# Kernel tuning notes

Hardware: AMD Instinct MI355X
Metric: run time of the kernel (lower is better)

Reference implementation:

```python
import jax, jax.numpy as jnp
import numpy as np

N = 50000          # nodes
E = 800000         # edges (no self loops; self loops added in reference)
D = 128            # in_channels == out_channels (required by index_add into x)
HEADS = 1
NEG_SLOPE = 0.2
NUM_LABELS = 7


def setup_inputs() -> dict:
    key = jax.random.key(0)
    k0, k1, k2, k3, k4, k5 = jax.random.split(key, 6)
    x = jax.random.normal(k0, (N, D), dtype=jnp.float32)
    # edges guaranteed self-loop-free (remove_self_loops is then a no-op)
    src = jax.random.randint(k1, (E,), 0, N, dtype=jnp.int32)
    off = jax.random.randint(k2, (E,), 1, N, dtype=jnp.int32)
    dst = (src + off) % N
    edge_index = jnp.stack([src, dst])  # [2, E]
    node_label = jax.random.randint(k3, (N,), 0, 8, dtype=jnp.int32)  # 0 = inactive, 1..7 active
    glorot = float(np.sqrt(6.0 / (D + D)))
    weight_id = jax.random.uniform(k4, (NUM_LABELS, D, D), jnp.float32, -glorot, glorot)
    ga = float(np.sqrt(6.0 / (HEADS * 2 * D + 1)))
    att = jax.random.uniform(k5, (1, HEADS, 2 * D), jnp.float32, -ga, ga)
    return {"x": x, "edge_index": edge_index, "node_label": node_label,
            "weight_id": weight_id, "att": att}


def reference(x, edge_index, node_label, weight_id, att):
    n, d = x.shape
    # --- per-label identity transform: ox = x + W_{label-1} x for labels 1..7 ---
    y = jnp.einsum('nd,kdo->nko', x, weight_id)           # [N, 7, D]
    valid = (node_label >= 1) & (node_label <= NUM_LABELS)
    idx = jnp.clip(node_label - 1, 0, NUM_LABELS - 1)
    delta = jnp.take_along_axis(y, idx[:, None, None], axis=1)[:, 0]  # [N, D]
    ox = x + jnp.where(valid[:, None], delta, jnp.zeros_like(delta))
    # --- add self loops (input has none) ---
    loops = jnp.arange(n, dtype=edge_index.dtype)
    src = jnp.concatenate([edge_index[0], loops])
    dst = jnp.concatenate([edge_index[1], loops])
    # --- GAT message: gather, attention score, edge softmax over dst ---
    x_j = ox[src].reshape(-1, HEADS, d)                   # [Et, 1, D]
    x_i = ox[dst].reshape(-1, HEADS, d)
    alpha = (x_i * att[:, :, :d]).sum(-1) + (x_j * att[:, :, d:]).sum(-1)  # [Et, 1]
    alpha = jax.nn.leaky_relu(alpha, NEG_SLOPE)
    amax = jax.ops.segment_max(alpha, dst, num_segments=n)  # every node has a self loop
    alpha = jnp.exp(alpha - amax[dst])
    denom = jax.ops.segment_sum(alpha, dst, num_segments=n)
    alpha = alpha / (denom[dst] + 1e-16)
    # dropout p=0 (eval) -> no-op
    msg = (x_j * alpha[:, :, None]).reshape(-1, HEADS * d)  # concat=True, heads=1
    out = jax.ops.segment_sum(msg, dst, num_segments=n)     # [N, D]; bias=False
    return out
```

## Files before the change

### kernel.cpp

```cpp
#include <hip/hip_runtime.h>
#include <math.h>

#define N_NODES 50000
#define N_EDGES 800000
#define DIM 128
#define DEG_CAP 48
#define BINS ((N_NODES + 255) / 256)
#define BIN_CAP 8192
#define EA_CHUNK 3125
#define BA_BLOCKS ((N_EDGES + EA_CHUNK - 1) / EA_CHUNK)
#define EA_UNR 13

#define LB_BLOCKS ((N_NODES + 255) / 256)
#define WT_BLOCKS ((7 * DIM * DIM + 255) / 256)
#define K1_GRID (BA_BLOCKS + LB_BLOCKS + WT_BLOCKS)

#define TR_TILES 3133
#define K2_GRID (BINS + TR_TILES)

#define XS_STRIDE 132

typedef __attribute__((ext_vector_type(8))) short short8;
typedef __attribute__((ext_vector_type(4))) float floatx4;

__device__ __forceinline__ unsigned short f2bf(float f) {
    unsigned int u = __float_as_uint(f);
    unsigned int r = (u + 0x7fff + ((u >> 16) & 1)) >> 16;
    return (unsigned short)r;
}
__device__ __forceinline__ float bf2f_lo(unsigned int v) { return __uint_as_float(v << 16); }
__device__ __forceinline__ float bf2f_hi(unsigned int v) { return __uint_as_float(v & 0xffff0000u); }

__global__ __launch_bounds__(256) void build_kernel(
        const int* __restrict__ src, const int* __restrict__ dst,
        const int* __restrict__ label, const float* __restrict__ W,
        unsigned short* __restrict__ Wt,
        int* __restrict__ bin_cur, unsigned int* __restrict__ binned,
        int* __restrict__ lab_cnt, int* __restrict__ node_list) {
    int t = threadIdx.x;
    int blk = blockIdx.x;

    if (blk < BA_BLOCKS) {
        __shared__ int hist[BINS], base_s[BINS], rank[BINS];
        for (int i = t; i < BINS; i += 256) { hist[i] = 0; rank[i] = 0; }
        __syncthreads();
        int e0 = blk * EA_CHUNK;
        int e1 = e0 + EA_CHUNK; if (e1 > N_EDGES) e1 = N_EDGES;
        int dl[EA_UNR];
        #pragma unroll
        for (int k = 0; k < EA_UNR; k++) {
            int e = e0 + t + k * 256;
            dl[k] = (e < e1) ? dst[e] : -1;
        }
        #pragma unroll
        for (int k = 0; k < EA_UNR; k++)
            if (dl[k] >= 0) atomicAdd(&hist[dl[k] >> 8], 1);
        __syncthreads();
        for (int i = t; i < BINS; i += 256)
            base_s[i] = (hist[i] > 0) ? atomicAdd(&bin_cur[i], hist[i]) : 0;
        __syncthreads();
        int sl[EA_UNR];
        #pragma unroll
        for (int k = 0; k < EA_UNR; k++) {
            int e = e0 + t + k * 256;
            sl[k] = (e < e1) ? src[e] : 0;
        }
        #pragma unroll
        for (int k = 0; k < EA_UNR; k++) {
            if (dl[k] >= 0) {
                int d = dl[k];
                int b = d >> 8;
                int r = atomicAdd(&rank[b], 1);
                int slot = base_s[b] + r;
                if (slot < BIN_CAP)
                    binned[(size_t)b * BIN_CAP + slot] = (unsigned int)(sl[k] | ((d & 255) << 16));
            }
        }
    } else if (blk < BA_BLOCKS + LB_BLOCKS) {
        __shared__ int lcnt[8], lbase[8], lrank[8];
        int i = (blk - BA_BLOCKS) * 256 + t;
        if (t < 8) { lcnt[t] = 0; lrank[t] = 0; }
        __syncthreads();
        int b = -1;
        if (i < N_NODES) {
            int lab = label[i];
            b = (lab >= 1 && lab <= 7) ? (lab - 1) : 7;
            atomicAdd(&lcnt[b], 1);
        }
        __syncthreads();
        if (t < 8) lbase[t] = (lcnt[t] > 0) ? atomicAdd(&lab_cnt[t], lcnt[t]) : 0;
        __syncthreads();
        if (i < N_NODES) {
            int r = atomicAdd(&lrank[b], 1);
            node_list[(size_t)b * N_NODES + lbase[b] + r] = i;
        }
    } else {
        int j = (blk - BA_BLOCKS - LB_BLOCKS) * 256 + t;
        if (j < 7 * DIM * DIM) {
            int b = j >> 14;
            int d = (j >> 7) & 127;
            int c = j & 127;
            Wt[((size_t)b * DIM + c) * DIM + d] = f2bf(W[j]);
        }
    }
}

__global__ __launch_bounds__(256) void phase2_kernel(
        const float* __restrict__ x, const float* __restrict__ att,
        const int* __restrict__ lab_cnt, const int* __restrict__ node_list,
        const unsigned short* __restrict__ Wt,
        const int* __restrict__ bin_cur, const unsigned int* __restrict__ binned,
        unsigned short* __restrict__ oxh, float* __restrict__ ai, float* __restrict__ aj,
        int* __restrict__ cnt, unsigned short* __restrict__ bucket) {
    __shared__ __align__(16) char smem[25600];
    int t = threadIdx.x;
    int blk = blockIdx.x;

    if (blk < BINS) {
        unsigned short (*rows)[DEG_CAP] = (unsigned short (*)[DEG_CAP])smem;
        int* lcnt = (int*)(smem + 24576);
        int b = blk;
        int m = bin_cur[b]; if (m > BIN_CAP) m = BIN_CAP;
        const unsigned int* bp = binned + (size_t)b * BIN_CAP;

        lcnt[t] = 0;
        __syncthreads();
        for (int i0 = 0; i0 < m; i0 += 1024) {
            unsigned int v[4];
            #pragma unroll
            for (int u = 0; u < 4; u++) {
                int i = i0 + u * 256 + t;
                v[u] = (i < m) ? bp[i] : 0u;
            }
            #pragma unroll
            for (int u = 0; u < 4; u++) {
                int i = i0 + u * 256 + t;
                if (i < m) {
                    int ln = (v[u] >> 16) & 255;
                    int p = atomicAdd(&lcnt[ln], 1);
                    if (p < DEG_CAP) rows[ln][p] = (unsigned short)(v[u] & 0xFFFF);
                }
            }
        }
        __syncthreads();
        int n = b * 256 + t;
        if (n < N_NODES) {
            int deg = lcnt[t];
            if (deg > DEG_CAP) deg = DEG_CAP;
            cnt[n] = deg;
        }
        uint4* gdst = (uint4*)(bucket + (size_t)b * 256 * DEG_CAP);
        const uint4* lsrc = (const uint4*)rows;
        #pragma unroll
        for (int k = 0; k < (256 * DEG_CAP * 2 / 16) / 256; k++)
            gdst[t + k * 256] = lsrc[t + k * 256];
    } else {
        int tile = blk - BINS;
        int b = 0, base = 0, tcnt = 0;
        for (; b < 8; b++) {
            int c = lab_cnt[b];
            int nt = (c + 15) >> 4;
            if (tile < nt) { base = b * N_NODES + tile * 16; tcnt = c - tile * 16; break; }
            tile -= nt;
        }
        if (b == 8) return;
        if (tcnt > 16) tcnt = 16;

        float* xs  = (float*)smem;
        float* red = (float*)(smem + 16 * XS_STRIDE * 4);

        {
            const float4* x4 = (const float4*)x;
            int j = t;
            #pragma unroll
            for (int k = 0; k < 2; k++, j += 256) {
                int row = j >> 5;
                int c4  = j & 31;
                int node = node_list[base + ((row < tcnt) ? row : 0)];
                float4 v = x4[(size_t)node * 32 + c4];
                *(float4*)(xs + row * XS_STRIDE + c4 * 4) = v;
            }
        }
        __syncthreads();

        int wv = t >> 6;
        int lane = t & 63;
        int m = lane & 15;
        int quad = lane >> 4;

        floatx4 acc[2];
        acc[0] = (floatx4){0.f, 0.f, 0.f, 0.f};
        acc[1] = (floatx4){0.f, 0.f, 0.f, 0.f};

        if (b < 7) {
            short8 afrag[4];
            #pragma unroll
            for (int kk = 0; kk < 4; kk++) {
                const float* xp = xs + m * XS_STRIDE + kk * 32 + quad * 8;
                short8 a;
                #pragma unroll
                for (int e = 0; e < 8; e++) a[e] = (short)f2bf(xp[e]);
                afrag[kk] = a;
            }
            const unsigned short* WtB = Wt + (size_t)b * DIM * DIM;
            #pragma unroll
            for (int kk = 0; kk < 4; kk++) {
                #pragma unroll
                for (int nl = 0; nl < 2; nl++) {
                    int c = wv * 32 + nl * 16 + m;
                    short8 bfrag = *(const short8*)(WtB + (size_t)c * DIM + kk * 32 + quad * 8);
                    acc[nl] = __builtin_amdgcn_mfma_f32_16x16x32_bf16(afrag[kk], bfrag, acc[nl], 0, 0, 0);
                }
            }
        }

        int nodes[4];
        #pragma unroll
        for (int r = 0; r < 4; r++) {
            int rw = quad * 4 + r;
            nodes[r] = node_list[base + ((rw < tcnt) ? rw : 0)];
        }
        float pi[4] = {0.f, 0.f, 0.f, 0.f};
        float pj[4] = {0.f, 0.f, 0.f, 0.f};
        #pragma unroll
        for (int nl = 0; nl < 2; nl++) {
            int c = wv * 32 + nl * 16 + m;
            float a1 = att[c];
            float a2 = att[DIM + c];
            #pragma unroll
            for (int r = 0; r < 4; r++) {
                int rw = quad * 4 + r;
                if (rw < tcnt) {
                    float xv = xs[rw * XS_STRIDE + c];
                    float v = (b < 7) ? (acc[nl][r] + xv) : xv;
                    oxh[(size_t)nodes[r] * DIM + c] = f2bf(v);
                    pi[r] += v * a1;
                    pj[r] += v * a2;
                }
            }
        }
        #pragma unroll
        for (int r = 0; r < 4; r++) {
            #pragma unroll
            for (int off = 1; off < 16; off <<= 1) {
                pi[r] += __shfl_xor(pi[r], off, 64);
                pj[r] += __shfl_xor(pj[r], off, 64);
            }
        }
        if (m == 0) {
            #pragma unroll
            for (int r = 0; r < 4; r++) {
                red[wv * 32 + quad * 4 + r]      = pi[r];
                red[wv * 32 + 16 + quad * 4 + r] = pj[r];
            }
        }
        __syncthreads();
        if (t < 16 && t < tcnt) {
            int node = node_list[base + t];
            float si = 0.f, sj = 0.f;
            #pragma unroll
            for (int w2 = 0; w2 < 4; w2++) {
                si += red[w2 * 32 + t];
                sj += red[w2 * 32 + 16 + t];
            }
            ai[node] = si;
            aj[node] = sj;
        }
    }
}

__global__ __launch_bounds__(256) void gather8_kernel(
        const int* __restrict__ cnt, const unsigned short* __restrict__ bucket,
        const float* __restrict__ ai, const float* __restrict__ aj,
        const uint4* __restrict__ tab,
        float* __restrict__ out) {
    __shared__ float wls[4][64];
    __shared__ int   sls[4][64];
    int wv = threadIdx.x >> 6;
    int lane = threadIdx.x & 63;
    int n = blockIdx.x * 4 + wv;
    int deg = cnt[n];
    if (deg > DEG_CAP) deg = DEG_CAP;
    const unsigned short* row = bucket + (size_t)n * DEG_CAP;
    float ain = ai[n];

    float a = -INFINITY;
    int s = n;
    if (lane < deg) {
        s = row[lane];
        a = ain + aj[s];
        a = (a > 0.0f) ? a : 0.2f * a;
    } else if (lane == deg) {
        a = ain + aj[n];
        a = (a > 0.0f) ? a : 0.2f * a;
    }
    float mx = a;
    #pragma unroll
    for (int off = 32; off > 0; off >>= 1) mx = fmaxf(mx, __shfl_xor(mx, off, 64));
    float w = expf(a - mx);
    float ssum = w;
    #pragma unroll
    for (int off = 32; off > 0; off >>= 1) ssum += __shfl_xor(ssum, off, 64);
    float wn = w / (ssum + 1e-16f);

    wls[wv][lane] = wn;
    sls[wv][lane] = s;
    __syncthreads();

    const float* wp = wls[wv];
    const int*   sp = sls[wv];
    float wsf = wp[deg];

    int g = lane >> 4;
    int cl = lane & 15;
    float ac0 = 0.f, ac1 = 0.f, ac2 = 0.f, ac3 = 0.f;
    float ac4 = 0.f, ac5 = 0.f, ac6 = 0.f, ac7 = 0.f;

    if (g == 0) {
        uint4 v = tab[(size_t)n * 16 + cl];
        ac0 += wsf * bf2f_lo(v.x); ac1 += wsf * bf2f_hi(v.x);
        ac2 += wsf * bf2f_lo(v.y); ac3 += wsf * bf2f_hi(v.y);
        ac4 += wsf * bf2f_lo(v.z); ac5 += wsf * bf2f_hi(v.z);
        ac6 += wsf * bf2f_lo(v.w); ac7 += wsf * bf2f_hi(v.w);
    }

    int niter = (deg + 3) >> 2;
    int k = 0;
    for (; k + 4 <= niter; k += 4) {
        int i0 = g + 4 * k, i1 = i0 + 4, i2 = i0 + 8, i3 = i0 + 12;
        float w0 = wp[i0]; int s0 = sp[i0];
        float w1 = wp[i1]; int s1 = sp[i1];
        float w2 = wp[i2]; int s2 = sp[i2];
        float w3 = wp[i3]; int s3 = sp[i3];
        if (i0 >= deg) w0 = 0.0f;
        if (i1 >= deg) w1 = 0.0f;
        if (i2 >= deg) w2 = 0.0f;
        if (i3 >= deg) w3 = 0.0f;
        uint4 v0 = tab[(size_t)s0 * 16 + cl];
        uint4 v1 = tab[(size_t)s1 * 16 + cl];
        uint4 v2 = tab[(size_t)s2 * 16 + cl];
        uint4 v3 = tab[(size_t)s3 * 16 + cl];
        ac0 += w0 * bf2f_lo(v0.x); ac1 += w0 * bf2f_hi(v0.x);
        ac2 += w0 * bf2f_lo(v0.y); ac3 += w0 * bf2f_hi(v0.y);
        ac4 += w0 * bf2f_lo(v0.z); ac5 += w0 * bf2f_hi(v0.z);
        ac6 += w0 * bf2f_lo(v0.w); ac7 += w0 * bf2f_hi(v0.w);
        ac0 += w1 * bf2f_lo(v1.x); ac1 += w1 * bf2f_hi(v1.x);
        ac2 += w1 * bf2f_lo(v1.y); ac3 += w1 * bf2f_hi(v1.y);
        ac4 += w1 * bf2f_lo(v1.z); ac5 += w1 * bf2f_hi(v1.z);
        ac6 += w1 * bf2f_lo(v1.w); ac7 += w1 * bf2f_hi(v1.w);
        ac0 += w2 * bf2f_lo(v2.x); ac1 += w2 * bf2f_hi(v2.x);
        ac2 += w2 * bf2f_lo(v2.y); ac3 += w2 * bf2f_hi(v2.y);
        ac4 += w2 * bf2f_lo(v2.z); ac5 += w2 * bf2f_hi(v2.z);
        ac6 += w2 * bf2f_lo(v2.w); ac7 += w2 * bf2f_hi(v2.w);
        ac0 += w3 * bf2f_lo(v3.x); ac1 += w3 * bf2f_hi(v3.x);
        ac2 += w3 * bf2f_lo(v3.y); ac3 += w3 * bf2f_hi(v3.y);
        ac4 += w3 * bf2f_lo(v3.z); ac5 += w3 * bf2f_hi(v3.z);
        ac6 += w3 * bf2f_lo(v3.w); ac7 += w3 * bf2f_hi(v3.w);
    }
    for (; k < niter; k++) {
        int i0 = g + 4 * k;
        float w0 = (i0 < deg) ? wp[i0] : 0.0f;
        int s0 = sp[i0];
        uint4 v0 = tab[(size_t)s0 * 16 + cl];
        ac0 += w0 * bf2f_lo(v0.x); ac1 += w0 * bf2f_hi(v0.x);
        ac2 += w0 * bf2f_lo(v0.y); ac3 += w0 * bf2f_hi(v0.y);
        ac4 += w0 * bf2f_lo(v0.z); ac5 += w0 * bf2f_hi(v0.z);
        ac6 += w0 * bf2f_lo(v0.w); ac7 += w0 * bf2f_hi(v0.w);
    }

    #pragma unroll
    for (int off = 16; off < 64; off <<= 1) {
        ac0 += __shfl_xor(ac0, off, 64); ac1 += __shfl_xor(ac1, off, 64);
        ac2 += __shfl_xor(ac2, off, 64); ac3 += __shfl_xor(ac3, off, 64);
        ac4 += __shfl_xor(ac4, off, 64); ac5 += __shfl_xor(ac5, off, 64);
        ac6 += __shfl_xor(ac6, off, 64); ac7 += __shfl_xor(ac7, off, 64);
    }
    if (g == 0) {
        float* op = out + (size_t)n * DIM + cl * 8;
        float4 o0; o0.x = ac0; o0.y = ac1; o0.z = ac2; o0.w = ac3;
        float4 o1; o1.x = ac4; o1.y = ac5; o1.z = ac6; o1.w = ac7;
        *(float4*)op = o0;
        *(float4*)(op + 4) = o1;
    }
}

extern "C" void kernel_launch(void* const* d_in, const int* in_sizes, int n_in,
                              void* d_out, int out_size, void* d_ws, size_t ws_size,
                              hipStream_t stream) {
    const float* x     = (const float*)d_in[0];
    const int*   ei    = (const int*)d_in[1];
    const int*   label = (const int*)d_in[2];
    const float* W     = (const float*)d_in[3];
    const float* att   = (const float*)d_in[4];
    float* out = (float*)d_out;

    const int* src = ei;
    const int* dst = ei + N_EDGES;

    char* w = (char*)d_ws;
    unsigned short* oxh    = (unsigned short*)w; w += sizeof(unsigned short) * (size_t)N_NODES * DIM;
    unsigned short* Wt     = (unsigned short*)w; w += sizeof(unsigned short) * 7 * DIM * DIM;
    unsigned short* bucket = (unsigned short*)w; w += sizeof(unsigned short) * (size_t)BINS * 256 * DEG_CAP;
    unsigned int*   binned = (unsigned int*)w;   w += sizeof(unsigned int) * (size_t)BINS * BIN_CAP;
    int*   cnt       = (int*)w;    w += sizeof(int) * N_NODES;
    int*   node_list = (int*)w;    w += sizeof(int) * (size_t)8 * N_NODES;
    float* ai        = (float*)w;  w += sizeof(float) * N_NODES;
    float* aj        = (float*)w;  w += sizeof(float) * N_NODES;
    int*   lab_cnt   = (int*)w;    w += sizeof(int) * 8;
    int*   bin_cur   = (int*)w;    w += sizeof(int) * BINS;

    hipMemsetAsync(lab_cnt, 0, sizeof(int) * (8 + BINS), stream);

    build_kernel<<<K1_GRID, 256, 0, stream>>>(src, dst, label, W,
                                              Wt, bin_cur, binned, lab_cnt, node_list);

    phase2_kernel<<<K2_GRID, 256, 0, stream>>>(x, att, lab_cnt, node_list, Wt,
                                               bin_cur, binned, oxh, ai, aj, cnt, bucket);

    gather8_kernel<<<(N_NODES + 3) / 4, 256, 0, stream>>>(cnt, bucket, ai, aj,
                                                          (const uint4*)oxh, out);
}
```

Measured before the change: 151.0 us.

## Process 32 nodes per transform tile and use packed bf16 conversion

The per-label transform tile grows from 16 to 32 nodes, with two MFMA subtiles per block. Each block loads the W fragments once into registers and reuses them for both subtiles, which halves the tile count and the W loads per node. Scalar float-to-bf16 rounding is replaced by the v_cvt_pk_bf16_f32 instruction, and the label counts are read into registers before the tile search. The cost is higher register use per thread and more shared memory for xs. The smem buffer size must hold 32 rows plus the larger reduction array, and that allocation is not visible here.

```diff
diff --git a/kernel.cpp b/kernel.cpp
--- a/kernel.cpp
+++ b/kernel.cpp
@@ -15,7 +15,7 @@
 #define WT_BLOCKS ((7 * DIM * DIM + 255) / 256)
 #define K1_GRID (BA_BLOCKS + LB_BLOCKS + WT_BLOCKS)
 
-#define TR_TILES 3133
+#define TR_TILES 1571
 #define K2_GRID (BINS + TR_TILES)
 
 #define XS_STRIDE 132
@@ -27,6 +27,11 @@
     unsigned int u = __float_as_uint(f);
     unsigned int r = (u + 0x7fff + ((u >> 16) & 1)) >> 16;
     return (unsigned short)r;
+}
+__device__ __forceinline__ unsigned int cvtpk_bf16(float lo, float hi) {
+    unsigned int r;
+    asm volatile("v_cvt_pk_bf16_f32 %0, %1, %2" : "=v"(r) : "v"(lo), "v"(hi));
+    return r;
 }
 __device__ __forceinline__ float bf2f_lo(unsigned int v) { return __uint_as_float(v << 16); }
 __device__ __forceinline__ float bf2f_hi(unsigned int v) { return __uint_as_float(v & 0xffff0000u); }
@@ -155,25 +160,30 @@
         for (int k = 0; k < (256 * DEG_CAP * 2 / 16) / 256; k++)
             gdst[t + k * 256] = lsrc[t + k * 256];
     } else {
+        int lc[8];
+        #pragma unroll
+        for (int q = 0; q < 8; q++) lc[q] = lab_cnt[q];
+
         int tile = blk - BINS;
         int b = 0, base = 0, tcnt = 0;
+        #pragma unroll
         for (; b < 8; b++) {
-            int c = lab_cnt[b];
-            int nt = (c + 15) >> 4;
-            if (tile < nt) { base = b * N_NODES + tile * 16; tcnt = c - tile * 16; break; }
+            int c = lc[b];
+            int nt = (c + 31) >> 5;
+            if (tile < nt) { base = b * N_NODES + tile * 32; tcnt = c - tile * 32; break; }
             tile -= nt;
         }
         if (b == 8) return;
-        if (tcnt > 16) tcnt = 16;
+        if (tcnt > 32) tcnt = 32;
 
         float* xs  = (float*)smem;
-        float* red = (float*)(smem + 16 * XS_STRIDE * 4);
+        float* red = (float*)(smem + 32 * XS_STRIDE * 4);
 
         {
             const float4* x4 = (const float4*)x;
             int j = t;
             #pragma unroll
-            for (int k = 0; k < 2; k++, j += 256) {
+            for (int k = 0; k < 4; k++, j += 256) {
                 int row = j >> 5;
                 int c4  = j & 31;
                 int node = node_list[base + ((row < tcnt) ? row : 0)];
@@ -188,80 +198,92 @@
         int m = lane & 15;
         int quad = lane >> 4;
 
-        floatx4 acc[2];
-        acc[0] = (floatx4){0.f, 0.f, 0.f, 0.f};
-        acc[1] = (floatx4){0.f, 0.f, 0.f, 0.f};
+        floatx4 acc[2][2];
+        #pragma unroll
+        for (int st = 0; st < 2; st++)
+            #pragma unroll
+            for (int nl = 0; nl < 2; nl++)
+                acc[st][nl] = (floatx4){0.f, 0.f, 0.f, 0.f};
 
         if (b < 7) {
-            short8 afrag[4];
-            #pragma unroll
-            for (int kk = 0; kk < 4; kk++) {
-                const float* xp = xs + m * XS_STRIDE + kk * 32 + quad * 8;
-                short8 a;
-                #pragma unroll
-                for (int e = 0; e < 8; e++) a[e] = (short)f2bf(xp[e]);
-                afrag[kk] = a;
-            }
+            short8 bfrag[4][2];
             const unsigned short* WtB = Wt + (size_t)b * DIM * DIM;
             #pragma unroll
-            for (int kk = 0; kk < 4; kk++) {
+            for (int kk = 0; kk < 4; kk++)
                 #pragma unroll
                 for (int nl = 0; nl < 2; nl++) {
                     int c = wv * 32 + nl * 16 + m;
-                    short8 bfrag = *(const short8*)(WtB + (size_t)c * DIM + kk * 32 + quad * 8);
-                    acc[nl] = __builtin_amdgcn_mfma_f32_16x16x32_bf16(afrag[kk], bfrag, acc[nl], 0, 0, 0);
-                }
-            }
-        }
-
-        int nodes[4];
-        #pragma unroll
-        for (int r = 0; r < 4; r++) {
-            int rw = quad * 4 + r;
-            nodes[r] = node_list[base + ((rw < tcnt) ? rw : 0)];
-        }
-        float pi[4] = {0.f, 0.f, 0.f, 0.f};
-        float pj[4] = {0.f, 0.f, 0.f, 0.f};
-        #pragma unroll
-        for (int nl = 0; nl < 2; nl++) {
-            int c = wv * 32 + nl * 16 + m;
-            float a1 = att[c];
-            float a2 = att[DIM + c];
+                    bfrag[kk][nl] = *(const short8*)(WtB + (size_t)c * DIM + kk * 32 + quad * 8);
+                }
+            #pragma unroll
+            for (int st = 0; st < 2; st++) {
+                #pragma unroll
+                for (int kk = 0; kk < 4; kk++) {
+                    const float* xp = xs + (st * 16 + m) * XS_STRIDE + kk * 32 + quad * 8;
+                    union { short8 s8; unsigned int u[4]; } a;
+                    a.u[0] = cvtpk_bf16(xp[0], xp[1]);
+                    a.u[1] = cvtpk_bf16(xp[2], xp[3]);
+                    a.u[2] = cvtpk_bf16(xp[4], xp[5]);
+                    a.u[3] = cvtpk_bf16(xp[6], xp[7]);
+                    #pragma unroll
+                    for (int nl = 0; nl < 2; nl++)
+                        acc[st][nl] = __builtin_amdgcn_mfma_f32_16x16x32_bf16(a.s8, bfrag[kk][nl], acc[st][nl], 0, 0, 0);
+                }
+            }
+        }
+
+        #pragma unroll
+        for (int st = 0; st < 2; st++) {
+            int nodes[4];
             #pragma unroll
             for (int r = 0; r < 4; r++) {
-                int rw = quad * 4 + r;
-                if (rw < tcnt) {
-                    float xv = xs[rw * XS_STRIDE + c];
-                    float v = (b < 7) ? (acc[nl][r] + xv) : xv;
-                    oxh[(size_t)nodes[r] * DIM + c] = f2bf(v);
-                    pi[r] += v * a1;
-                    pj[r] += v * a2;
-                }
-            }
-        }
-        #pragma unroll
-        for (int r = 0; r < 4; r++) {
-            #pragma unroll
-            for (int off = 1; off < 16; off <<= 1) {
-                pi[r] += __shfl_xor(pi[r], off, 64);
-                pj[r] += __shfl_xor(pj[r], off, 64);
-            }
-        }
-        if (m == 0) {
+                int rw = st * 16 + quad * 4 + r;
+                nodes[r] = node_list[base + ((rw < tcnt) ? rw : 0)];
+            }
+            float pi[4] = {0.f, 0.f, 0.f, 0.f};
+            float pj[4] = {0.f, 0.f, 0.f, 0.f};
+            #pragma unroll
+            for (int nl = 0; nl < 2; nl++) {
+                int c = wv * 32 + nl * 16 + m;
+                float a1 = att[c];
+                float a2 = att[DIM + c];
+                #pragma unroll
+                for (int r = 0; r < 4; r++) {
+                    int rw = st * 16 + quad * 4 + r;
+                    if (rw < tcnt) {
+                        float xv = xs[rw * XS_STRIDE + c];
+                        float v = (b < 7) ? (acc[st][nl][r] + xv) : xv;
+                        oxh[(size_t)nodes[r] * DIM + c] = (unsigned short)(cvtpk_bf16(v, v) & 0xffff);
+                        pi[r] += v * a1;
+                        pj[r] += v * a2;
+                    }
+                }
+            }
             #pragma unroll
             for (int r = 0; r < 4; r++) {
-                red[wv * 32 + quad * 4 + r]      = pi[r];
-                red[wv * 32 + 16 + quad * 4 + r] = pj[r];
-            }
-        }
-        __syncthreads();
-        if (t < 16 && t < tcnt) {
+                #pragma unroll
+                for (int off = 1; off < 16; off <<= 1) {
+                    pi[r] += __shfl_xor(pi[r], off, 64);
+                    pj[r] += __shfl_xor(pj[r], off, 64);
+                }
+            }
+            if (m == 0) {
+                #pragma unroll
+                for (int r = 0; r < 4; r++) {
+                    int node32 = st * 16 + quad * 4 + r;
+                    red[wv * 64 + node32]      = pi[r];
+                    red[wv * 64 + 32 + node32] = pj[r];
+                }
+            }
+        }
+        __syncthreads();
+        if (t < 32 && t < tcnt) {
             int node = node_list[base + t];
             float si = 0.f, sj = 0.f;
             #pragma unroll
             for (int w2 = 0; w2 < 4; w2++) {
-                si += red[w2 * 32 + t];
-                sj += red[w2 * 32 + 16 + t];
+                si += red[w2 * 64 + t];
+                sj += red[w2 * 64 + 32 + t];
             }
             ai[node] = si;
             aj[node] = sj;
```

New measurement: 147.2 us, median of 2. -2.6%, faster.
